# Kernel optimization log

Hardware: AMD Instinct MI355X
Metric: run time of the kernel (lower is better)

## Reference

```python
import jax, jax.numpy as jnp
import numpy as np

NI = 627   # num_inputs (hardcoded 627 in original forward)
NH = 1024  # num_hidden
EPS_BN = 1e-5

def get_mask(in_f, out_f, nf, mask_type=None):
    in_deg = np.arange(in_f) % nf
    out_deg = np.arange(out_f) % nf
    if mask_type == 'output':
        out_deg = out_deg - 1
    return jnp.asarray((out_deg[:, None] >= in_deg[None, :]).astype(np.float32))

M_IN = get_mask(NI, NH, NI, 'input')        # [NH, NI]
M_H = get_mask(NH, NH, NI)                  # [NH, NH]
M_OUT = get_mask(NH, 2 * NI, NI, 'output')  # [2*NI, NH]

def masked_linear(x, W, b, mask):
    return x @ (W * mask).T + b

def conv1x1(x, W, b):
    # x: [B,C,L], W: [O,C] (kernel_size=1 conv == pointwise channel mix)
    return jnp.einsum('bcl,oc->bol', x, W) + b[None, :, None]

def bn_train(x, g, b):
    # BatchNorm1d training-mode: biased batch stats over (N, L)
    m = x.mean(axis=(0, 2), keepdims=True)
    v = x.var(axis=(0, 2), keepdims=True)
    return (x - m) * jax.lax.rsqrt(v + EPS_BN) * g[None, :, None] + b[None, :, None]

def setup_inputs() -> dict:
    key = jax.random.key(0)
    ks = iter(jax.random.split(key, 32))
    B = 512
    inputs = jax.random.randint(next(ks), (B, NI), 0, 300).astype(jnp.float32)
    def lin(k, o, i):
        return jax.random.normal(k, (o, i), jnp.float32) / np.sqrt(i)
    d = {'inputs': inputs}
    d['W_in'] = lin(next(ks), NH, NI); d['b_in'] = jnp.zeros((NH,), jnp.float32)
    d['W_h1'] = lin(next(ks), NH, NH); d['b_h1'] = jnp.zeros((NH,), jnp.float32)
    d['W_h2'] = lin(next(ks), NH, NH); d['b_h2'] = jnp.zeros((NH,), jnp.float32)
    d['W_out'] = lin(next(ks), 2 * NI, NH); d['b_out'] = jnp.zeros((2 * NI,), jnp.float32)
    chans = [(90, 1), (180, 90), (180, 180), (180, 180), (300, 180)]
    for idx, (o, c) in enumerate(chans, 1):
        d[f'cw{idx}'] = lin(next(ks), o, c)
        d[f'cb{idx}'] = jnp.zeros((o,), jnp.float32)
        if idx < 5:
            d[f'g{idx}'] = jnp.ones((o,), jnp.float32)
            d[f'be{idx}'] = jnp.zeros((o,), jnp.float32)
    return d

def reference(inputs, W_in, b_in, W_h1, b_h1, W_h2, b_h2, W_out, b_out,
              cw1, cb1, g1, be1, cw2, cb2, g2, be2, cw3, cb3, g3, be3,
              cw4, cb4, g4, be4, cw5, cb5):
    # MADE joiner + trunk (trunk = [act, ML, act, ML, ML_out])
    h = masked_linear(inputs, W_in, b_in, M_IN)
    h = jax.nn.relu(h)
    h = masked_linear(h, W_h1, b_h1, M_H)
    h = jax.nn.relu(h)
    h = masked_linear(h, W_h2, b_h2, M_H)
    out = masked_linear(h, W_out, b_out, M_OUT)      # [B, 2*NI]
    gamma_raw, theta = jnp.split(out, 2, axis=1)
    gamma = jax.nn.sigmoid(gamma_raw[:, 2:])          # [B, NI-2]
    # 1x1-conv / BN / ReLU trunk over theta viewed as [B,1,NI]
    x = theta[:, None, :]
    x = jax.nn.relu(bn_train(conv1x1(x, cw1, cb1), g1, be1))
    x = jax.nn.relu(bn_train(conv1x1(x, cw2, cb2), g2, be2))
    x = jax.nn.relu(bn_train(conv1x1(x, cw3, cb3), g3, be3))
    x = jax.nn.relu(bn_train(conv1x1(x, cw4, cb4), g4, be4))
    pred = conv1x1(x, cw5, cb5)                       # [B, 300, NI]
    logp = jax.nn.log_softmax(pred, axis=1)
    tgt = inputs.astype(jnp.int32)                    # [B, NI] class ids
    nll = -jnp.take_along_axis(logp, tgt[:, None, :], axis=1)[:, 0, :]  # [B, NI]
    ll = jnp.where(inputs[:, 2:] > 0,
                   0.1 * jnp.log(gamma + 1e-10) - nll[:, 2:],
                   0.1 * jnp.log(1.0 - gamma + 1e-10)).sum(axis=-1, keepdims=True)
    # mean cross-entropy over first two pixels (scalar, default reduction='mean')
    ll = ll - nll[:, :2].mean()
    return ll
```

## Files before the change

### kernel.cpp

```cpp
#include <hip/hip_runtime.h>
#include <hip/hip_bf16.h>
#include <math.h>

#define BATCH 512
#define NI 627
#define NH 1024
#define NOUTF 1254
#define LLEN 627
#define NBL (512 * 627)
#define EPSBN 1e-5f
#define NSLOT 10240
#define NRED2 40
#define NRED34 20

typedef __attribute__((ext_vector_type(8))) short bf16x8;
typedef __attribute__((ext_vector_type(4))) float f32x4;
typedef unsigned int uint32;
typedef unsigned short ushort16;

__device__ inline short f2b(float x) {
  __hip_bfloat16 h = __float2bfloat16(x);
  return *reinterpret_cast<short*>(&h);
}
__device__ inline float b2f(short s) {
  return __uint_as_float(((uint32)(ushort16)s) << 16);
}
__device__ inline f32x4 mfma16(bf16x8 a, bf16x8 b, f32x4 c) {
  return __builtin_amdgcn_mfma_f32_16x16x32_bf16(a, b, c, 0, 0, 0);
}
__device__ inline bf16x8 zero8() {
  bf16x8 z;
#pragma unroll
  for (int i = 0; i < 8; ++i) z[i] = 0;
  return z;
}
__device__ inline bf16x8 buildx1r(float4 alo, float4 ahi, float4 blo, float4 bhi, float th) {
  bf16x8 r;
  r[0] = f2b(fmaxf(fmaf(alo.x, th, blo.x), 0.f));
  r[1] = f2b(fmaxf(fmaf(alo.y, th, blo.y), 0.f));
  r[2] = f2b(fmaxf(fmaf(alo.z, th, blo.z), 0.f));
  r[3] = f2b(fmaxf(fmaf(alo.w, th, blo.w), 0.f));
  r[4] = f2b(fmaxf(fmaf(ahi.x, th, bhi.x), 0.f));
  r[5] = f2b(fmaxf(fmaf(ahi.y, th, bhi.y), 0.f));
  r[6] = f2b(fmaxf(fmaf(ahi.z, th, bhi.z), 0.f));
  r[7] = f2b(fmaxf(fmaf(ahi.w, th, bhi.w), 0.f));
  return r;
}
__device__ inline bf16x8 buildx1(const float* __restrict__ A1v, const float* __restrict__ B1v,
                                 int k0, float th) {
  float4 alo = *reinterpret_cast<const float4*>(&A1v[k0]);
  float4 ahi = *reinterpret_cast<const float4*>(&A1v[k0 + 4]);
  float4 blo = *reinterpret_cast<const float4*>(&B1v[k0]);
  float4 bhi = *reinterpret_cast<const float4*>(&B1v[k0 + 4]);
  return buildx1r(alo, ahi, blo, bhi, th);
}

__device__ inline void prep_mlpw_elem(const float* W, short* Wb, int i,
                                      int Nreal, int Kreal, int Kpad, int mode) {
  int n = i / Kpad, k = i - n * Kpad;
  float w = 0.f;
  if (n < Nreal && k < Kreal) {
    int od = n >= 627 ? n - 627 : n;
    int kd = k >= 627 ? k - 627 : k;
    bool keep = (mode == 0) ? (od >= k) : (mode == 1) ? (od >= kd) : (od > kd);
    if (keep) w = W[n * Kreal + k];
  }
  Wb[i] = f2b(w);
}
__device__ inline void prep_convw_elem(const float* W, short* Wb, int i,
                                       int Oreal, int Kreal, int Kpad) {
  int o = i / Kpad, k = i - o * Kpad;
  Wb[i] = (o < Oreal && k < Kreal) ? f2b(W[o * Kreal + k]) : (short)0;
}

#define PB_INB   1280
#define PB_WB1   (PB_INB + 2560)
#define PB_WB2   (PB_WB1 + 4096)
#define PB_WB3   (PB_WB2 + 4096)
#define PB_WB4   (PB_WB3 + 5120)
#define PB_CW2   (PB_WB4 + 72)
#define PB_CW3   (PB_CW2 + 144)
#define PB_CW4   (PB_CW3 + 144)
#define PB_CW5   (PB_CW4 + 240)
#define PB_CB    (PB_CW5 + 2)

__global__ __launch_bounds__(256) void prep_all(
    const float* __restrict__ inputs, short* __restrict__ INB,
    const float* __restrict__ W_in, short* __restrict__ WB1,
    const float* __restrict__ W_h1, short* __restrict__ WB2,
    const float* __restrict__ W_h2, short* __restrict__ WB3,
    const float* __restrict__ W_out, short* __restrict__ WB4,
    const float* __restrict__ cw2, short* __restrict__ CW2B,
    const float* __restrict__ cw3, short* __restrict__ CW3B,
    const float* __restrict__ cw4, short* __restrict__ CW4B,
    const float* __restrict__ cw5, short* __restrict__ CW5B,
    const float* __restrict__ cb2, const float* __restrict__ cb3,
    const float* __restrict__ cb4, const float* __restrict__ cb5,
    float* __restrict__ cb2p, float* __restrict__ cb3p,
    float* __restrict__ cb4p, float* __restrict__ cb5p)
{
  const int bid = blockIdx.x;
  if (bid < PB_INB) {
    int i = bid * 256 + threadIdx.x;
    if (i < 512 * 640) {
      int m = i / 640, k = i - m * 640;
      INB[i] = (k < NI) ? f2b(inputs[m * NI + k]) : (short)0;
    }
  } else if (bid < PB_WB1) {
    int i = (bid - PB_INB) * 256 + threadIdx.x;
    if (i < 1024 * 640) prep_mlpw_elem(W_in, WB1, i, 1024, 627, 640, 0);
  } else if (bid < PB_WB2) {
    int i = (bid - PB_WB1) * 256 + threadIdx.x;
    prep_mlpw_elem(W_h1, WB2, i, 1024, 1024, 1024, 1);
  } else if (bid < PB_WB3) {
    int i = (bid - PB_WB2) * 256 + threadIdx.x;
    prep_mlpw_elem(W_h2, WB3, i, 1024, 1024, 1024, 1);
  } else if (bid < PB_WB4) {
    int i = (bid - PB_WB3) * 256 + threadIdx.x;
    if (i < 1280 * 1024) prep_mlpw_elem(W_out, WB4, i, 1254, 1024, 1024, 2);
  } else if (bid < PB_CW2) {
    int i = (bid - PB_WB4) * 256 + threadIdx.x;
    if (i < 192 * 96) prep_convw_elem(cw2, CW2B, i, 180, 90, 96);
  } else if (bid < PB_CW3) {
    int i = (bid - PB_CW2) * 256 + threadIdx.x;
    if (i < 192 * 192) prep_convw_elem(cw3, CW3B, i, 180, 180, 192);
  } else if (bid < PB_CW4) {
    int i = (bid - PB_CW3) * 256 + threadIdx.x;
    if (i < 192 * 192) prep_convw_elem(cw4, CW4B, i, 180, 180, 192);
  } else if (bid < PB_CW5) {
    int i = (bid - PB_CW4) * 256 + threadIdx.x;
    if (i < 320 * 192) prep_convw_elem(cw5, CW5B, i, 300, 180, 192);
  } else {
    int c = (bid - PB_CW5) * 256 + threadIdx.x;
    if (c < 192) {
      cb2p[c] = (c < 180) ? cb2[c] : 0.f;
      cb3p[c] = (c < 180) ? cb3[c] : 0.f;
      cb4p[c] = (c < 180) ? cb4[c] : 0.f;
    }
    if (c < 320) cb5p[c] = (c < 300) ? cb5[c] : 0.f;
  }
}

template<int KPAD>
__global__ __launch_bounds__(256) void mlp_mfma(
    const short* __restrict__ A, const short* __restrict__ Wb, const float* __restrict__ bias,
    float* __restrict__ Cf, short* __restrict__ Cb, int Nreal, int relu)
{
  __shared__ float red[2][2][2][4][64];
  const int tid = threadIdx.x;
  const int l = tid & 63, wv = tid >> 6;
  const int wn = wv >> 1, kh = wv & 1;
  const int m0 = blockIdx.y * 32;
  const int n0 = blockIdx.x * 64 + wn * 32;
  const int lr = l & 15, lk = (l >> 4) * 8, lm4 = (l >> 4) * 4;
  f32x4 acc[2][2] = {};
  constexpr int khalf = KPAD >> 1;
  constexpr int nk = khalf >> 5;
#pragma unroll
  for (int ks = 0; ks < nk; ++ks) {
    int k0 = kh * khalf + ks * 32 + lk;
    bf16x8 a0 = *reinterpret_cast<const bf16x8*>(&A[(size_t)(m0 + lr) * KPAD + k0]);
    bf16x8 a1 = *reinterpret_cast<const bf16x8*>(&A[(size_t)(m0 + 16 + lr) * KPAD + k0]);
    bf16x8 b0 = *reinterpret_cast<const bf16x8*>(&Wb[(size_t)(n0 + lr) * KPAD + k0]);
    bf16x8 b1 = *reinterpret_cast<const bf16x8*>(&Wb[(size_t)(n0 + 16 + lr) * KPAD + k0]);
    acc[0][0] = mfma16(a0, b0, acc[0][0]);
    acc[0][1] = mfma16(a0, b1, acc[0][1]);
    acc[1][0] = mfma16(a1, b0, acc[1][0]);
    acc[1][1] = mfma16(a1, b1, acc[1][1]);
  }
  if (kh == 1) {
#pragma unroll
    for (int mi = 0; mi < 2; ++mi)
#pragma unroll
      for (int nj = 0; nj < 2; ++nj)
#pragma unroll
        for (int r = 0; r < 4; ++r) red[wn][mi][nj][r][l] = acc[mi][nj][r];
  }
  __syncthreads();
  if (kh == 0) {
#pragma unroll
    for (int mi = 0; mi < 2; ++mi)
#pragma unroll
      for (int nj = 0; nj < 2; ++nj) {
        int n = n0 + nj * 16 + lr;
        if (n >= Nreal) continue;
        float bi = bias[n];
#pragma unroll
        for (int r = 0; r < 4; ++r) {
          int m = m0 + mi * 16 + lm4 + r;
          float v = acc[mi][nj][r] + red[wn][mi][nj][r][l] + bi;
          if (relu) v = fmaxf(v, 0.f);
          if (Cb) Cb[(size_t)m * Nreal + n] = f2b(v);
          else Cf[(size_t)m * Nreal + n] = v;
        }
      }
  }
}

__global__ __launch_bounds__(256) void theta_stats(const float* __restrict__ outb, float* __restrict__ tstat)
{
  int b = blockIdx.x;
  const float* th = outb + (size_t)b * NOUTF + NI;
  float s = 0.f, q = 0.f;
  for (int l = threadIdx.x; l < LLEN; l += 256) { float t = th[l]; s += t; q += t * t; }
  for (int off = 1; off < 64; off <<= 1) { s += __shfl_xor(s, off); q += __shfl_xor(q, off); }
  __shared__ float tmp[8];
  int w = threadIdx.x >> 6;
  if ((threadIdx.x & 63) == 0) { tmp[w] = s; tmp[4 + w] = q; }
  __syncthreads();
  if (threadIdx.x == 0) {
    atomicAdd(&tstat[0], tmp[0] + tmp[1] + tmp[2] + tmp[3]);
    atomicAdd(&tstat[1], tmp[4] + tmp[5] + tmp[6] + tmp[7]);
  }
}

__global__ void finalize_conv1(const float* __restrict__ tstat, const float* __restrict__ cw1,
                               const float* __restrict__ g1, const float* __restrict__ be1,
                               float* __restrict__ a1, float* __restrict__ b1)
{
  int c = threadIdx.x;
  if (c >= 96) return;
  if (c < 90) {
    float mt = tstat[0] / (float)NBL;
    float vt = tstat[1] / (float)NBL - mt * mt;
    float w = cw1[c];
    float rs = rsqrtf(w * w * vt + EPSBN);
    float a = w * g1[c] * rs;
    a1[c] = a;
    b1[c] = be1[c] - a * mt;
  } else { a1[c] = 0.f; b1[c] = 0.f; }
}

__global__ __launch_bounds__(192) void bn_reduce1(const float* __restrict__ Sp, const float* __restrict__ Qp,
                                                  float* __restrict__ Sred, float* __restrict__ Qred)
{
  int c = threadIdx.x;
  if (c >= 180) return;
  int base = blockIdx.x * 256;
  float s = 0.f, q = 0.f;
  for (int r = 0; r < 256; ++r) {
    s += Sp[(size_t)(base + r) * 180 + c];
    q += Qp[(size_t)(base + r) * 180 + c];
  }
  Sred[blockIdx.x * 180 + c] = s;
  Qred[blockIdx.x * 180 + c] = q;
}

__global__ void finalize_bn2(const float* __restrict__ Sred, const float* __restrict__ Qred,
                             const float* __restrict__ g, const float* __restrict__ be,
                             float* __restrict__ aP, float* __restrict__ bP, int nred)
{
  int c = threadIdx.x;
  if (c >= 192) return;
  if (c < 180) {
    float s = 0.f, q = 0.f;
    for (int p = 0; p < nred; ++p) { s += Sred[p * 180 + c]; q += Qred[p * 180 + c]; }
    float m = s / (float)NBL;
    float v = q / (float)NBL - m * m;
    float a = g[c] * rsqrtf(v + EPSBN);
    aP[c] = a;
    bP[c] = be[c] - m * a;
  } else { aP[c] = 0.f; bP[c] = 0.f; }
}

__global__ __launch_bounds__(512) void conv2_stats(
    const float* __restrict__ OUTB, const float* __restrict__ A1v, const float* __restrict__ B1v,
    const short* __restrict__ cw2b, const float* __restrict__ cb2p,
    float* __restrict__ Sp, float* __restrict__ Qp)
{
  const int tid = threadIdx.x;
  const int b = blockIdx.y, j0 = blockIdx.x * 128;
  const int l = tid & 63, wv = tid >> 6, wm = wv >> 2, wn = wv & 3;
  const int lr = l & 15, lk = (l >> 4) * 8, lm4 = (l >> 4) * 4;
  const int jj0 = j0 + wn * 32 + lr, jj1 = jj0 + 16;
  const float th0 = (jj0 < LLEN) ? OUTB[(size_t)b * NOUTF + NI + jj0] : 0.f;
  const float th1 = (jj1 < LLEN) ? OUTB[(size_t)b * NOUTF + NI + jj1] : 0.f;
  f32x4 acc[6][2] = {};
#pragma unroll
  for (int ks = 0; ks < 3; ++ks) {
    int k0 = ks * 32 + lk;
    bf16x8 b0 = buildx1(A1v, B1v, k0, th0);
    bf16x8 b1 = buildx1(A1v, B1v, k0, th1);
#pragma unroll
    for (int mi = 0; mi < 6; ++mi) {
      bf16x8 av = *reinterpret_cast<const bf16x8*>(&cw2b[(wm * 96 + mi * 16 + lr) * 96 + k0]);
      acc[mi][0] = mfma16(av, b0, acc[mi][0]);
      acc[mi][1] = mfma16(av, b1, acc[mi][1]);
    }
  }
  const size_t slot = (size_t)(blockIdx.y * gridDim.x + blockIdx.x) * 4 + wn;
#pragma unroll
  for (int mi = 0; mi < 6; ++mi) {
    int m0c = wm * 96 + mi * 16 + lm4;
    float s4[4] = {0.f, 0.f, 0.f, 0.f}, q4[4] = {0.f, 0.f, 0.f, 0.f};
#pragma unroll
    for (int nj = 0; nj < 2; ++nj) {
      int jj = j0 + wn * 32 + nj * 16 + lr;
      if (jj < LLEN) {
#pragma unroll
        for (int r = 0; r < 4; ++r) {
          float v = acc[mi][nj][r] + cb2p[m0c + r];
          s4[r] += v; q4[r] += v * v;
        }
      }
    }
#pragma unroll
    for (int off = 1; off < 16; off <<= 1)
#pragma unroll
      for (int r = 0; r < 4; ++r) { s4[r] += __shfl_xor(s4[r], off); q4[r] += __shfl_xor(q4[r], off); }
    if (lr == 0) {
#pragma unroll
      for (int r = 0; r < 4; ++r) {
        int o = m0c + r;
        if (o < 180) {
          Sp[slot * 180 + o] = s4[r];
          Qp[slot * 180 + o] = q4[r];
        }
      }
    }
  }
}

__global__ __launch_bounds__(512) void fused_conv23(
    const float* __restrict__ OUTB, const float* __restrict__ A1v, const float* __restrict__ B1v,
    const short* __restrict__ cw2b, const float* __restrict__ cb2p,
    const float* __restrict__ a2, const float* __restrict__ b2,
    const short* __restrict__ cw3b, const float* __restrict__ cb3p,
    short* __restrict__ Y, float* __restrict__ Sp, float* __restrict__ Qp)
{
  __shared__ short wl2[192][98];
  __shared__ short wl3[192][196];
  __shared__ short xT2[128][196];
  const int tid = threadIdx.x;
  const int b = blockIdx.x;
  for (int t = tid; t < 192 * 12; t += 512) {
    int row = t / 12, c8 = (t - row * 12) * 8;
    *reinterpret_cast<bf16x8*>(&wl2[row][c8]) = *reinterpret_cast<const bf16x8*>(&cw2b[row * 96 + c8]);
  }
  for (int t = tid; t < 192 * 24; t += 512) {
    int row = t / 24, c8 = (t - row * 24) * 8;
    *reinterpret_cast<bf16x8*>(&wl3[row][c8]) = *reinterpret_cast<const bf16x8*>(&cw3b[row * 192 + c8]);
  }
  const int l = tid & 63, wv = tid >> 6, wm = wv >> 1, wn = wv & 1;
  const int lr = l & 15, lk = (l >> 4) * 8, lm4 = (l >> 4) * 4;
  float a2r[3][4], f2r[3][4], cb3r[3][4];
#pragma unroll
  for (int mi = 0; mi < 3; ++mi)
#pragma unroll
    for (int r = 0; r < 4; ++r) {
      int c = wm * 48 + mi * 16 + lm4 + r;
      float a = a2[c];
      a2r[mi][r] = a;
      f2r[mi][r] = fmaf(a, cb2p[c], b2[c]);
      cb3r[mi][r] = cb3p[c];
    }
  __syncthreads();
  for (int tile = 0; tile < 5; ++tile) {
    const int j0 = tile * 128;
    float th[4];
#pragma unroll
    for (int nj = 0; nj < 4; ++nj) {
      int jj = j0 + wn * 64 + nj * 16 + lr;
      th[nj] = (jj < LLEN) ? OUTB[(size_t)b * NOUTF + NI + jj] : 0.f;
    }
    f32x4 acc[3][4] = {};
#pragma unroll
    for (int ks = 0; ks < 3; ++ks) {
      int k0 = ks * 32 + lk;
      float4 alo = *reinterpret_cast<const float4*>(&A1v[k0]);
      float4 ahi = *reinterpret_cast<const float4*>(&A1v[k0 + 4]);
      float4 blo = *reinterpret_cast<const float4*>(&B1v[k0]);
      float4 bhi = *reinterpret_cast<const float4*>(&B1v[k0 + 4]);
      bf16x8 bb[4];
#pragma unroll
      for (int nj = 0; nj < 4; ++nj) bb[nj] = buildx1r(alo, ahi, blo, bhi, th[nj]);
      bf16x8 av[3];
#pragma unroll
      for (int mi = 0; mi < 3; ++mi)
        av[mi] = *reinterpret_cast<const bf16x8*>(&wl2[wm * 48 + mi * 16 + lr][k0]);
#pragma unroll
      for (int mi = 0; mi < 3; ++mi)
#pragma unroll
        for (int nj = 0; nj < 4; ++nj)
          acc[mi][nj] = mfma16(av[mi], bb[nj], acc[mi][nj]);
    }
    __syncthreads();
#pragma unroll
    for (int mi = 0; mi < 3; ++mi) {
      int m0c = wm * 48 + mi * 16 + lm4;
#pragma unroll
      for (int nj = 0; nj < 4; ++nj) {
        int col = wn * 64 + nj * 16 + lr;
        float x0 = fmaxf(fmaf(a2r[mi][0], acc[mi][nj][0], f2r[mi][0]), 0.f);
        float x1 = fmaxf(fmaf(a2r[mi][1], acc[mi][nj][1], f2r[mi][1]), 0.f);
        float x2 = fmaxf(fmaf(a2r[mi][2], acc[mi][nj][2], f2r[mi][2]), 0.f);
        float x3 = fmaxf(fmaf(a2r[mi][3], acc[mi][nj][3], f2r[mi][3]), 0.f);
        uint2 w2;
        w2.x = (uint32)(ushort16)f2b(x0) | ((uint32)(ushort16)f2b(x1) << 16);
        w2.y = (uint32)(ushort16)f2b(x2) | ((uint32)(ushort16)f2b(x3) << 16);
        *reinterpret_cast<uint2*>(&xT2[col][m0c]) = w2;
      }
    }
    __syncthreads();
    f32x4 acc2[3][4] = {};
#pragma unroll
    for (int ks = 0; ks < 6; ++ks) {
      int k0 = ks * 32 + lk;
      bf16x8 bb[4];
#pragma unroll
      for (int nj = 0; nj < 4; ++nj)
        bb[nj] = *reinterpret_cast<const bf16x8*>(&xT2[wn * 64 + nj * 16 + lr][k0]);
      bf16x8 av[3];
#pragma unroll
      for (int mi = 0; mi < 3; ++mi)
        av[mi] = *reinterpret_cast<const bf16x8*>(&wl3[wm * 48 + mi * 16 + lr][k0]);
#pragma unroll
      for (int mi = 0; mi < 3; ++mi)
#pragma unroll
        for (int nj = 0; nj < 4; ++nj)
          acc2[mi][nj] = mfma16(av[mi], bb[nj], acc2[mi][nj]);
    }
    __syncthreads();
    const size_t slot = ((size_t)b * 5 + tile) * 2 + wn;
#pragma unroll
    for (int mi = 0; mi < 3; ++mi) {
      int m0c = wm * 48 + mi * 16 + lm4;
      float s4[4] = {0.f, 0.f, 0.f, 0.f}, q4[4] = {0.f, 0.f, 0.f, 0.f};
#pragma unroll
      for (int nj = 0; nj < 4; ++nj) {
        int col = wn * 64 + nj * 16 + lr;
        int jj = j0 + col;
        float v0 = acc2[mi][nj][0] + cb3r[mi][0];
        float v1 = acc2[mi][nj][1] + cb3r[mi][1];
        float v2 = acc2[mi][nj][2] + cb3r[mi][2];
        float v3 = acc2[mi][nj][3] + cb3r[mi][3];
        if (jj < LLEN) {
          s4[0] += v0; q4[0] += v0 * v0;
          s4[1] += v1; q4[1] += v1 * v1;
          s4[2] += v2; q4[2] += v2 * v2;
          s4[3] += v3; q4[3] += v3 * v3;
        }
        uint2 w2;
        w2.x = (uint32)(ushort16)f2b(v0) | ((uint32)(ushort16)f2b(v1) << 16);
        w2.y = (uint32)(ushort16)f2b(v2) | ((uint32)(ushort16)f2b(v3) << 16);
        *reinterpret_cast<uint2*>(&xT2[col][m0c]) = w2;
      }
#pragma unroll
      for (int off = 1; off < 16; off <<= 1)
#pragma unroll
        for (int r = 0; r < 4; ++r) { s4[r] += __shfl_xor(s4[r], off); q4[r] += __shfl_xor(q4[r], off); }
      if (lr == 0) {
#pragma unroll
        for (int r = 0; r < 4; ++r) {
          int o = m0c + r;
          if (o < 180) {
            Sp[slot * 180 + o] = s4[r];
            Qp[slot * 180 + o] = q4[r];
          }
        }
      }
    }
    __syncthreads();
    for (int f = tid; f < 128 * 24; f += 512) {
      int row = f / 24, c0 = (f - row * 24) * 8;
      int jj = j0 + row;
      if (jj < LLEN) {
        bf16x8 v = *reinterpret_cast<const bf16x8*>(&xT2[row][c0]);
        *reinterpret_cast<bf16x8*>(&Y[((size_t)b * 627 + jj) * 192 + c0]) = v;
      }
    }
  }
}

__global__ __launch_bounds__(512) void conv4_ip(
    short* __restrict__ Y, const float* __restrict__ a3, const float* __restrict__ b3,
    const short* __restrict__ cw4b, const float* __restrict__ cb4p,
    float* __restrict__ Sp, float* __restrict__ Qp)
{
  __shared__ short wl4[192][196];
  __shared__ short xT[128][196];
  const int tid = threadIdx.x;
  const int b = blockIdx.x;
  for (int t = tid; t < 192 * 24; t += 512) {
    int row = t / 24, c8 = (t - row * 24) * 8;
    *reinterpret_cast<bf16x8*>(&wl4[row][c8]) = *reinterpret_cast<const bf16x8*>(&cw4b[row * 192 + c8]);
  }
  const int l = tid & 63, wv = tid >> 6, wm = wv >> 1, wn = wv & 1;
  const int lr = l & 15, lk = (l >> 4) * 8, lm4 = (l >> 4) * 4;
  float cb4r[3][4];
#pragma unroll
  for (int mi = 0; mi < 3; ++mi)
#pragma unroll
    for (int r = 0; r < 4; ++r)
      cb4r[mi][r] = cb4p[wm * 48 + mi * 16 + lm4 + r];
  for (int tile = 0; tile < 5; ++tile) {
    const int j0 = tile * 128;
    __syncthreads();
    for (int t = tid; t < 128 * 24; t += 512) {
      int col = t / 24, oct = t - col * 24;
      int jj = j0 + col;
      int c0 = oct * 8;
      bf16x8 pk;
      if (jj < LLEN) {
        bf16x8 raw = *reinterpret_cast<const bf16x8*>(&Y[((size_t)b * 627 + jj) * 192 + c0]);
        float4 alo = *reinterpret_cast<const float4*>(&a3[c0]);
        float4 ahi = *reinterpret_cast<const float4*>(&a3[c0 + 4]);
        float4 blo = *reinterpret_cast<const float4*>(&b3[c0]);
        float4 bhi = *reinterpret_cast<const float4*>(&b3[c0 + 4]);
        pk[0] = f2b(fmaxf(fmaf(alo.x, b2f(raw[0]), blo.x), 0.f));
        pk[1] = f2b(fmaxf(fmaf(alo.y, b2f(raw[1]), blo.y), 0.f));
        pk[2] = f2b(fmaxf(fmaf(alo.z, b2f(raw[2]), blo.z), 0.f));
        pk[3] = f2b(fmaxf(fmaf(alo.w, b2f(raw[3]), blo.w), 0.f));
        pk[4] = f2b(fmaxf(fmaf(ahi.x, b2f(raw[4]), bhi.x), 0.f));
        pk[5] = f2b(fmaxf(fmaf(ahi.y, b2f(raw[5]), bhi.y), 0.f));
        pk[6] = f2b(fmaxf(fmaf(ahi.z, b2f(raw[6]), bhi.z), 0.f));
        pk[7] = f2b(fmaxf(fmaf(ahi.w, b2f(raw[7]), bhi.w), 0.f));
      } else {
        pk = zero8();
      }
      *reinterpret_cast<bf16x8*>(&xT[col][c0]) = pk;
    }
    __syncthreads();
    f32x4 acc[3][4] = {};
#pragma unroll
    for (int ks = 0; ks < 6; ++ks) {
      int k0 = ks * 32 + lk;
      bf16x8 bb[4];
#pragma unroll
      for (int nj = 0; nj < 4; ++nj)
        bb[nj] = *reinterpret_cast<const bf16x8*>(&xT[wn * 64 + nj * 16 + lr][k0]);
      bf16x8 av[3];
#pragma unroll
      for (int mi = 0; mi < 3; ++mi)
        av[mi] = *reinterpret_cast<const bf16x8*>(&wl4[wm * 48 + mi * 16 + lr][k0]);
#pragma unroll
      for (int mi = 0; mi < 3; ++mi)
#pragma unroll
        for (int nj = 0; nj < 4; ++nj)
          acc[mi][nj] = mfma16(av[mi], bb[nj], acc[mi][nj]);
    }
    __syncthreads();
    const size_t slot = ((size_t)b * 5 + tile) * 2 + wn;
#pragma unroll
    for (int mi = 0; mi < 3; ++mi) {
      int m0c = wm * 48 + mi * 16 + lm4;
      float s4[4] = {0.f, 0.f, 0.f, 0.f}, q4[4] = {0.f, 0.f, 0.f, 0.f};
#pragma unroll
      for (int nj = 0; nj < 4; ++nj) {
        int col = wn * 64 + nj * 16 + lr;
        int jj = j0 + col;
        float v0 = acc[mi][nj][0] + cb4r[mi][0];
        float v1 = acc[mi][nj][1] + cb4r[mi][1];
        float v2 = acc[mi][nj][2] + cb4r[mi][2];
        float v3 = acc[mi][nj][3] + cb4r[mi][3];
        if (jj < LLEN) {
          s4[0] += v0; q4[0] += v0 * v0;
          s4[1] += v1; q4[1] += v1 * v1;
          s4[2] += v2; q4[2] += v2 * v2;
          s4[3] += v3; q4[3] += v3 * v3;
        }
        uint2 w2;
        w2.x = (uint32)(ushort16)f2b(v0) | ((uint32)(ushort16)f2b(v1) << 16);
        w2.y = (uint32)(ushort16)f2b(v2) | ((uint32)(ushort16)f2b(v3) << 16);
        *reinterpret_cast<uint2*>(&xT[col][m0c]) = w2;
      }
#pragma unroll
      for (int off = 1; off < 16; off <<= 1)
#pragma unroll
        for (int r = 0; r < 4; ++r) { s4[r] += __shfl_xor(s4[r], off); q4[r] += __shfl_xor(q4[r], off); }
      if (lr == 0) {
#pragma unroll
        for (int r = 0; r < 4; ++r) {
          int o = m0c + r;
          if (o < 180) {
            Sp[slot * 180 + o] = s4[r];
            Qp[slot * 180 + o] = q4[r];
          }
        }
      }
    }
    __syncthreads();
    for (int f = tid; f < 128 * 24; f += 512) {
      int row = f / 24, c0 = (f - row * 24) * 8;
      int jj = j0 + row;
      if (jj < LLEN) {
        bf16x8 v = *reinterpret_cast<const bf16x8*>(&xT[row][c0]);
        *reinterpret_cast<bf16x8*>(&Y[((size_t)b * 627 + jj) * 192 + c0]) = v;
      }
    }
  }
}

__global__ __launch_bounds__(512) void conv5_nll(
    const short* __restrict__ Y, const float* __restrict__ a4, const float* __restrict__ b4,
    const short* __restrict__ cw5b, const float* __restrict__ cb5p,
    const float* __restrict__ inputs, float* __restrict__ nll)
{
  __shared__ short wlds[320][200];
  __shared__ short xT[64][200];
  __shared__ int tga[640];
  __shared__ float wmax[4][64];
  __shared__ float wsum[4][64];
  __shared__ float ptgt[64];
  const int tid = threadIdx.x;
  const int b = blockIdx.x;
  for (int t = tid; t < 320 * 24; t += 512) {
    int row = t / 24, c8 = (t - row * 24) * 8;
    *reinterpret_cast<bf16x8*>(&wlds[row][c8]) =
        *reinterpret_cast<const bf16x8*>(&cw5b[row * 192 + c8]);
  }
  for (int t = tid; t < 640; t += 512)
    tga[t] = (t < LLEN) ? (int)inputs[(size_t)b * NI + t] : 0;
  const int l = tid & 63, wv = tid >> 6;
  const int wm = wv >> 1, wn = wv & 1;
  const int lr = l & 15, lk = (l >> 4) * 8, lm4 = (l >> 4) * 4;
  const int mf0 = wm * 5;
  float aa[3][8], bb4[3][8];
#pragma unroll
  for (int s = 0; s < 3; ++s) {
    int t = tid + s * 512;
    int c8 = (t % 24) * 8;
#pragma unroll
    for (int i = 0; i < 8; ++i) { aa[s][i] = a4[c8 + i]; bb4[s][i] = b4[c8 + i]; }
  }
  float cbr[5][4];
#pragma unroll
  for (int mi = 0; mi < 5; ++mi)
#pragma unroll
    for (int r = 0; r < 4; ++r)
      cbr[mi][r] = cb5p[(mf0 + mi) * 16 + lm4 + r];
  bf16x8 raw[3];
#pragma unroll
  for (int s = 0; s < 3; ++s) {
    int t = tid + s * 512;
    int col = t / 24, c8 = (t - col * 24) * 8;
    raw[s] = (col < LLEN) ? *reinterpret_cast<const bf16x8*>(&Y[((size_t)b * 627 + col) * 192 + c8]) : zero8();
  }
  __syncthreads();
  for (int tile = 0; tile < 10; ++tile) {
    const int l0 = tile * 64;
#pragma unroll
    for (int s = 0; s < 3; ++s) {
      int t = tid + s * 512;
      int col = t / 24, c8 = (t - col * 24) * 8;
      bf16x8 pk;
#pragma unroll
      for (int i = 0; i < 8; ++i)
        pk[i] = f2b(fmaxf(fmaf(aa[s][i], b2f(raw[s][i]), bb4[s][i]), 0.f));
      *reinterpret_cast<bf16x8*>(&xT[col][c8]) = pk;
    }
    __syncthreads();
    f32x4 acc[5][2] = {};
#pragma unroll
    for (int ks = 0; ks < 6; ++ks) {
      int k0 = ks * 32 + lk;
      bf16x8 bb0 = *reinterpret_cast<const bf16x8*>(&xT[wn * 32 + lr][k0]);
      bf16x8 bb1 = *reinterpret_cast<const bf16x8*>(&xT[wn * 32 + 16 + lr][k0]);
#pragma unroll
      for (int mi = 0; mi < 5; ++mi) {
        bf16x8 av = *reinterpret_cast<const bf16x8*>(&wlds[(mf0 + mi) * 16 + lr][k0]);
        acc[mi][0] = mfma16(av, bb0, acc[mi][0]);
        acc[mi][1] = mfma16(av, bb1, acc[mi][1]);
      }
    }
    if (tile < 9) {
#pragma unroll
      for (int s = 0; s < 3; ++s) {
        int t = tid + s * 512;
        int col = t / 24, c8 = (t - col * 24) * 8;
        int jj = l0 + 64 + col;
        raw[s] = (jj < LLEN) ? *reinterpret_cast<const bf16x8*>(&Y[((size_t)b * 627 + jj) * 192 + c8]) : zero8();
      }
    }
    float vmax0 = -1e30f, vmax1 = -1e30f;
    int t0 = tga[l0 + wn * 32 + lr], t1 = tga[l0 + wn * 32 + 16 + lr];
#pragma unroll
    for (int mi = 0; mi < 5; ++mi) {
#pragma unroll
      for (int r = 0; r < 4; ++r) {
        int m = (mf0 + mi) * 16 + lm4 + r;
        bool ok = (m < 300);
        float v0 = ok ? (acc[mi][0][r] + cbr[mi][r]) : -1e30f;
        float v1 = ok ? (acc[mi][1][r] + cbr[mi][r]) : -1e30f;
        acc[mi][0][r] = v0;
        acc[mi][1][r] = v1;
        vmax0 = fmaxf(vmax0, v0);
        vmax1 = fmaxf(vmax1, v1);
        if (m == t0) ptgt[wn * 32 + lr] = v0;
        if (m == t1) ptgt[wn * 32 + 16 + lr] = v1;
      }
    }
    vmax0 = fmaxf(vmax0, __shfl_xor(vmax0, 16)); vmax0 = fmaxf(vmax0, __shfl_xor(vmax0, 32));
    vmax1 = fmaxf(vmax1, __shfl_xor(vmax1, 16)); vmax1 = fmaxf(vmax1, __shfl_xor(vmax1, 32));
    if (l < 16) { wmax[wm][wn * 32 + lr] = vmax0; wmax[wm][wn * 32 + 16 + lr] = vmax1; }
    __syncthreads();
    float gmax0, gmax1;
    {
      int c0c = wn * 32 + lr, c1c = wn * 32 + 16 + lr;
      gmax0 = fmaxf(fmaxf(wmax[0][c0c], wmax[1][c0c]), fmaxf(wmax[2][c0c], wmax[3][c0c]));
      gmax1 = fmaxf(fmaxf(wmax[0][c1c], wmax[1][c1c]), fmaxf(wmax[2][c1c], wmax[3][c1c]));
    }
    float vs0 = 0.f, vs1 = 0.f;
#pragma unroll
    for (int mi = 0; mi < 5; ++mi)
#pragma unroll
      for (int r = 0; r < 4; ++r) {
        vs0 += __expf(acc[mi][0][r] - gmax0);
        vs1 += __expf(acc[mi][1][r] - gmax1);
      }
    vs0 += __shfl_xor(vs0, 16); vs0 += __shfl_xor(vs0, 32);
    vs1 += __shfl_xor(vs1, 16); vs1 += __shfl_xor(vs1, 32);
    if (l < 16) { wsum[wm][wn * 32 + lr] = vs0; wsum[wm][wn * 32 + 16 + lr] = vs1; }
    __syncthreads();
    if (tid < 64) {
      int jj = l0 + tid;
      if (jj < LLEN) {
        float gm = fmaxf(fmaxf(wmax[0][tid], wmax[1][tid]), fmaxf(wmax[2][tid], wmax[3][tid]));
        float gs = wsum[0][tid] + wsum[1][tid] + wsum[2][tid] + wsum[3][tid];
        nll[(size_t)b * LLEN + jj] = gm + logf(gs) - ptgt[tid];
      }
    }
  }
}

__global__ __launch_bounds__(256) void ll_pass1(
    const float* __restrict__ outb, const float* __restrict__ nll,
    const float* __restrict__ inputs, float* __restrict__ llp, float* __restrict__ sc)
{
  int b = blockIdx.x;
  float s = 0.f;
  for (int l = 2 + (int)threadIdx.x; l < LLEN; l += 256) {
    float graw = outb[(size_t)b * NOUTF + l];
    float sg = 1.f / (1.f + expf(-graw));
    float term;
    if (inputs[(size_t)b * NI + l] > 0.f)
      term = 0.1f * logf(sg + 1e-10f) - nll[(size_t)b * LLEN + l];
    else
      term = 0.1f * logf(1.f - sg + 1e-10f);
    s += term;
  }
  for (int off = 1; off < 64; off <<= 1) s += __shfl_xor(s, off);
  __shared__ float tmp[4];
  if ((threadIdx.x & 63) == 0) tmp[threadIdx.x >> 6] = s;
  __syncthreads();
  if (threadIdx.x == 0) {
    llp[b] = tmp[0] + tmp[1] + tmp[2] + tmp[3];
    atomicAdd(sc, nll[(size_t)b * LLEN] + nll[(size_t)b * LLEN + 1]);
  }
}

__global__ void ll_pass2(const float* __restrict__ llp, const float* __restrict__ sc, float* __restrict__ outp)
{
  int i = blockIdx.x * blockDim.x + threadIdx.x;
  if (i < BATCH) outp[i] = llp[i] - sc[0] * (1.f / 1024.f);
}

extern "C" void kernel_launch(void* const* d_in, const int* in_sizes, int n_in,
                              void* d_out, int out_size, void* d_ws, size_t ws_size,
                              hipStream_t stream)
{
  const float* inputs = (const float*)d_in[0];
  const float* W_in = (const float*)d_in[1];
  const float* b_in = (const float*)d_in[2];
  const float* W_h1 = (const float*)d_in[3];
  const float* b_h1 = (const float*)d_in[4];
  const float* W_h2 = (const float*)d_in[5];
  const float* b_h2 = (const float*)d_in[6];
  const float* W_out = (const float*)d_in[7];
  const float* b_out = (const float*)d_in[8];
  const float* cw1 = (const float*)d_in[9];
  const float* g1 = (const float*)d_in[11];
  const float* be1 = (const float*)d_in[12];
  const float* cw2 = (const float*)d_in[13];
  const float* cb2 = (const float*)d_in[14];
  const float* g2 = (const float*)d_in[15];
  const float* be2 = (const float*)d_in[16];
  const float* cw3 = (const float*)d_in[17];
  const float* cb3 = (const float*)d_in[18];
  const float* g3 = (const float*)d_in[19];
  const float* be3 = (const float*)d_in[20];
  const float* cw4 = (const float*)d_in[21];
  const float* cb4 = (const float*)d_in[22];
  const float* g4 = (const float*)d_in[23];
  const float* be4 = (const float*)d_in[24];
  const float* cw5 = (const float*)d_in[25];
  const float* cb5 = (const float*)d_in[26];

  char* p = (char*)d_ws;
  short* Y = (short*)p;    p += (size_t)512 * 627 * 192 * 2;
  short* INB = (short*)p;  p += (size_t)512 * 640 * 2;
  short* HB1 = (short*)p;  p += (size_t)512 * 1024 * 2;
  short* HB2 = (short*)p;  p += (size_t)512 * 1024 * 2;
  short* HB3 = (short*)p;  p += (size_t)512 * 1024 * 2;
  short* WB1 = (short*)p;  p += (size_t)1024 * 640 * 2;
  short* WB2 = (short*)p;  p += (size_t)1024 * 1024 * 2;
  short* WB3 = (short*)p;  p += (size_t)1024 * 1024 * 2;
  short* WB4 = (short*)p;  p += (size_t)1280 * 1024 * 2;
  short* CW2B = (short*)p; p += (size_t)192 * 96 * 2;
  short* CW3B = (short*)p; p += (size_t)192 * 192 * 2;
  short* CW4B = (short*)p; p += (size_t)192 * 192 * 2;
  short* CW5B = (short*)p; p += (size_t)320 * 192 * 2;
  float* fp = (float*)p;
  float* OUTB = fp;  fp += (size_t)512 * 1254;
  float* NLLB = fp;  fp += 321028;
  float* LLP = fp;   fp += 512;
  float* A1 = fp;    fp += 96;
  float* B1g = fp;   fp += 96;
  float* A2 = fp;    fp += 192;
  float* B2g = fp;   fp += 192;
  float* A3 = fp;    fp += 192;
  float* B3g = fp;   fp += 192;
  float* A4 = fp;    fp += 192;
  float* B4g = fp;   fp += 192;
  float* CB2P = fp;  fp += 192;
  float* CB3P = fp;  fp += 192;
  float* CB4P = fp;  fp += 192;
  float* CB5P = fp;  fp += 320;
  float* TST = fp;   fp += 2;
  float* SC = fp;    fp += 2;
  float* SPP = fp;   fp += (size_t)NSLOT * 180;
  float* QPP = fp;   fp += (size_t)NSLOT * 180;
  float* SRED = fp;  fp += NRED2 * 180;
  float* QRED = fp;  fp += NRED2 * 180;

  hipMemsetAsync(TST, 0, 4 * sizeof(float), stream);

  prep_all<<<dim3(PB_CB), 256, 0, stream>>>(
      inputs, INB, W_in, WB1, W_h1, WB2, W_h2, WB3, W_out, WB4,
      cw2, CW2B, cw3, CW3B, cw4, CW4B, cw5, CW5B,
      cb2, cb3, cb4, cb5, CB2P, CB3P, CB4P, CB5P);

  mlp_mfma<640><<<dim3(16, 16), 256, 0, stream>>>(INB, WB1, b_in, nullptr, HB1, 1024, 1);
  mlp_mfma<1024><<<dim3(16, 16), 256, 0, stream>>>(HB1, WB2, b_h1, nullptr, HB2, 1024, 1);
  mlp_mfma<1024><<<dim3(16, 16), 256, 0, stream>>>(HB2, WB3, b_h2, nullptr, HB3, 1024, 0);
  mlp_mfma<1024><<<dim3(20, 16), 256, 0, stream>>>(HB3, WB4, b_out, OUTB, nullptr, 1254, 0);

  theta_stats<<<dim3(BATCH), 256, 0, stream>>>(OUTB, TST);
  finalize_conv1<<<1, 96, 0, stream>>>(TST, cw1, g1, be1, A1, B1g);

  conv2_stats<<<dim3(5, BATCH), 512, 0, stream>>>(OUTB, A1, B1g, CW2B, CB2P, SPP, QPP);
  bn_reduce1<<<dim3(NRED2), 192, 0, stream>>>(SPP, QPP, SRED, QRED);
  finalize_bn2<<<1, 192, 0, stream>>>(SRED, QRED, g2, be2, A2, B2g, NRED2);

  fused_conv23<<<dim3(BATCH), 512, 0, stream>>>(OUTB, A1, B1g, CW2B, CB2P, A2, B2g, CW3B, CB3P, Y, SPP, QPP);
  bn_reduce1<<<dim3(NRED34), 192, 0, stream>>>(SPP, QPP, SRED, QRED);
  finalize_bn2<<<1, 192, 0, stream>>>(SRED, QRED, g3, be3, A3, B3g, NRED34);

  conv4_ip<<<dim3(BATCH), 512, 0, stream>>>(Y, A3, B3g, CW4B, CB4P, SPP, QPP);
  bn_reduce1<<<dim3(NRED34), 192, 0, stream>>>(SPP, QPP, SRED, QRED);
  finalize_bn2<<<1, 192, 0, stream>>>(SRED, QRED, g4, be4, A4, B4g, NRED34);

  conv5_nll<<<dim3(BATCH), 512, 0, stream>>>(Y, A4, B4g, CW5B, CB5P, inputs, NLLB);

  ll_pass1<<<dim3(BATCH), 256, 0, stream>>>(OUTB, NLLB, inputs, LLP, SC);
  ll_pass2<<<dim3(2), 256, 0, stream>>>(LLP, SC, (float*)d_out);
}
```

Baseline: 519.3 us.

## Fuse ll_pass1 into conv5 NLL kernel and use online softmax merge

Folds the per-row log-likelihood reduction into the conv5/log-softmax kernel, so NLL values stay in shared memory and are no longer written to and reread from global memory, and one kernel launch goes away. Each wave's partial exp-sum now uses its own max and the block merges the partials with rescaling, which removes one __syncthreads per column tile. The cost is a little more shared memory and a few extra exps per column.

```diff
diff --git a/kernel.cpp b/kernel.cpp
--- a/kernel.cpp
+++ b/kernel.cpp
@@ -591,10 +591,11 @@
   }
 }
 
-__global__ __launch_bounds__(512) void conv5_nll(
+__global__ __launch_bounds__(512) void conv5_nll_ll(
     const short* __restrict__ Y, const float* __restrict__ a4, const float* __restrict__ b4,
     const short* __restrict__ cw5b, const float* __restrict__ cb5p,
-    const float* __restrict__ inputs, float* __restrict__ nll)
+    const float* __restrict__ inputs, const float* __restrict__ outb,
+    float* __restrict__ llp, float* __restrict__ sc)
 {
   __shared__ short wlds[320][200];
   __shared__ short xT[64][200];
@@ -602,6 +603,7 @@
   __shared__ float wmax[4][64];
   __shared__ float wsum[4][64];
   __shared__ float ptgt[64];
+  __shared__ float nlls[640];
   const int tid = threadIdx.x;
   const int b = blockIdx.x;
   for (int t = tid; t < 320 * 24; t += 512) {
@@ -692,60 +694,50 @@
     }
     vmax0 = fmaxf(vmax0, __shfl_xor(vmax0, 16)); vmax0 = fmaxf(vmax0, __shfl_xor(vmax0, 32));
     vmax1 = fmaxf(vmax1, __shfl_xor(vmax1, 16)); vmax1 = fmaxf(vmax1, __shfl_xor(vmax1, 32));
-    if (l < 16) { wmax[wm][wn * 32 + lr] = vmax0; wmax[wm][wn * 32 + 16 + lr] = vmax1; }
-    __syncthreads();
-    float gmax0, gmax1;
-    {
-      int c0c = wn * 32 + lr, c1c = wn * 32 + 16 + lr;
-      gmax0 = fmaxf(fmaxf(wmax[0][c0c], wmax[1][c0c]), fmaxf(wmax[2][c0c], wmax[3][c0c]));
-      gmax1 = fmaxf(fmaxf(wmax[0][c1c], wmax[1][c1c]), fmaxf(wmax[2][c1c], wmax[3][c1c]));
-    }
     float vs0 = 0.f, vs1 = 0.f;
 #pragma unroll
     for (int mi = 0; mi < 5; ++mi)
 #pragma unroll
       for (int r = 0; r < 4; ++r) {
-        vs0 += __expf(acc[mi][0][r] - gmax0);
-        vs1 += __expf(acc[mi][1][r] - gmax1);
+        vs0 += __expf(acc[mi][0][r] - vmax0);
+        vs1 += __expf(acc[mi][1][r] - vmax1);
       }
     vs0 += __shfl_xor(vs0, 16); vs0 += __shfl_xor(vs0, 32);
     vs1 += __shfl_xor(vs1, 16); vs1 += __shfl_xor(vs1, 32);
-    if (l < 16) { wsum[wm][wn * 32 + lr] = vs0; wsum[wm][wn * 32 + 16 + lr] = vs1; }
+    if (l < 16) {
+      wmax[wm][wn * 32 + lr] = vmax0; wmax[wm][wn * 32 + 16 + lr] = vmax1;
+      wsum[wm][wn * 32 + lr] = vs0;   wsum[wm][wn * 32 + 16 + lr] = vs1;
+    }
     __syncthreads();
     if (tid < 64) {
       int jj = l0 + tid;
       if (jj < LLEN) {
-        float gm = fmaxf(fmaxf(wmax[0][tid], wmax[1][tid]), fmaxf(wmax[2][tid], wmax[3][tid]));
-        float gs = wsum[0][tid] + wsum[1][tid] + wsum[2][tid] + wsum[3][tid];
-        nll[(size_t)b * LLEN + jj] = gm + logf(gs) - ptgt[tid];
-      }
-    }
-  }
-}
-
-__global__ __launch_bounds__(256) void ll_pass1(
-    const float* __restrict__ outb, const float* __restrict__ nll,
-    const float* __restrict__ inputs, float* __restrict__ llp, float* __restrict__ sc)
-{
-  int b = blockIdx.x;
+        float m0 = wmax[0][tid], m1 = wmax[1][tid], m2 = wmax[2][tid], m3 = wmax[3][tid];
+        float gm = fmaxf(fmaxf(m0, m1), fmaxf(m2, m3));
+        float gs = wsum[0][tid] * __expf(m0 - gm) + wsum[1][tid] * __expf(m1 - gm)
+                 + wsum[2][tid] * __expf(m2 - gm) + wsum[3][tid] * __expf(m3 - gm);
+        nlls[jj] = gm + logf(gs) - ptgt[tid];
+      }
+    }
+  }
+  __syncthreads();
   float s = 0.f;
-  for (int l = 2 + (int)threadIdx.x; l < LLEN; l += 256) {
-    float graw = outb[(size_t)b * NOUTF + l];
+  for (int lidx = 2 + tid; lidx < LLEN; lidx += 512) {
+    float graw = outb[(size_t)b * NOUTF + lidx];
     float sg = 1.f / (1.f + expf(-graw));
-    float term;
-    if (inputs[(size_t)b * NI + l] > 0.f)
-      term = 0.1f * logf(sg + 1e-10f) - nll[(size_t)b * LLEN + l];
-    else
-      term = 0.1f * logf(1.f - sg + 1e-10f);
+    float term = (tga[lidx] > 0) ? (0.1f * logf(sg + 1e-10f) - nlls[lidx])
+                                 : (0.1f * logf(1.f - sg + 1e-10f));
     s += term;
   }
   for (int off = 1; off < 64; off <<= 1) s += __shfl_xor(s, off);
-  __shared__ float tmp[4];
-  if ((threadIdx.x & 63) == 0) tmp[threadIdx.x >> 6] = s;
+  if (l == 0) wmax[0][wv] = s;
   __syncthreads();
-  if (threadIdx.x == 0) {
-    llp[b] = tmp[0] + tmp[1] + tmp[2] + tmp[3];
-    atomicAdd(sc, nll[(size_t)b * LLEN] + nll[(size_t)b * LLEN + 1]);
+  if (tid == 0) {
+    float tot = 0.f;
+#pragma unroll
+    for (int w = 0; w < 8; ++w) tot += wmax[0][w];
+    llp[b] = tot;
+    atomicAdd(sc, nlls[0] + nlls[1]);
   }
 }
 
@@ -822,6 +814,7 @@
   float* QPP = fp;   fp += (size_t)NSLOT * 180;
   float* SRED = fp;  fp += NRED2 * 180;
   float* QRED = fp;  fp += NRED2 * 180;
+  (void)NLLB;
 
   hipMemsetAsync(TST, 0, 4 * sizeof(float), stream);
 
@@ -850,8 +843,7 @@
   bn_reduce1<<<dim3(NRED34), 192, 0, stream>>>(SPP, QPP, SRED, QRED);
   finalize_bn2<<<1, 192, 0, stream>>>(SRED, QRED, g4, be4, A4, B4g, NRED34);
 
-  conv5_nll<<<dim3(BATCH), 512, 0, stream>>>(Y, A4, B4g, CW5B, CB5P, inputs, NLLB);
-
-  ll_pass1<<<dim3(BATCH), 256, 0, stream>>>(OUTB, NLLB, inputs, LLP, SC);
+  conv5_nll_ll<<<dim3(BATCH), 512, 0, stream>>>(Y, A4, B4g, CW5B, CB5P, inputs, OUTB, LLP, SC);
+
   ll_pass2<<<dim3(2), 256, 0, stream>>>(LLP, SC, (float*)d_out);
 }
```

Measured after the change: 505.1 us (median of 2 runs). -2.7%, faster.
